# Kernel optimization log

Hardware: AMD Instinct MI355X
Metric: run time of the kernel (lower is better)

Reference implementation:

```python
import jax, jax.numpy as jnp
import numpy as np

B, CIN, COUT, K, ADIM, H, W = 32, 64, 64, 3, 64, 128, 128
PAD = K // 2


def setup_inputs() -> dict:
    key = jax.random.key(0)
    ks = jax.random.split(key, 8)
    s = lambda fan: 1.0 / np.sqrt(fan)
    return {
        "x": jax.random.normal(ks[0], (B, CIN, H, W), dtype=jnp.float32),
        "base_w": jax.random.uniform(ks[1], (COUT, CIN, K, K), minval=-s(CIN * K * K), maxval=s(CIN * K * K), dtype=jnp.float32),
        "base_b": jax.random.uniform(ks[2], (COUT,), minval=-s(CIN * K * K), maxval=s(CIN * K * K), dtype=jnp.float32),
        "w1": jax.random.uniform(ks[3], (CIN, ADIM), minval=-s(CIN), maxval=s(CIN), dtype=jnp.float32),
        "b1": jax.random.uniform(ks[4], (ADIM,), minval=-s(CIN), maxval=s(CIN), dtype=jnp.float32),
        "w2": jax.random.uniform(ks[5], (ADIM, COUT * CIN * K * K), minval=-s(ADIM), maxval=s(ADIM), dtype=jnp.float32),
        "b2": jax.random.uniform(ks[6], (COUT * CIN * K * K,), minval=-s(ADIM), maxval=s(ADIM), dtype=jnp.float32),
        "scale": jnp.float32(0.1),
    }


def reference(x, base_w, base_b, w1, b1, w2, b2, scale):
    # adaptation net: global avg pool -> MLP -> tanh
    pooled = jnp.mean(x, axis=(2, 3))                              # [B, Cin]
    h = jax.nn.relu(pooled @ w1 + b1)                              # [B, adim]
    a = jnp.tanh(h @ w2 + b2).reshape(B, COUT, CIN, K, K)          # [B,Cout,Cin,K,K]
    adapted = base_w[None] + scale * a                             # per-sample weights

    def conv_one(xi, wi):
        # xi: [Cin,H,W], wi: [Cout,Cin,K,K]
        out = jax.lax.conv_general_dilated(
            xi[None], wi, window_strides=(1, 1),
            padding=[(PAD, PAD), (PAD, PAD)],
            dimension_numbers=("NCHW", "OIHW", "NCHW"))
        return out[0]

    y = jax.vmap(conv_one)(x, adapted)                             # [B,Cout,H,W]
    return y + base_b[None, :, None, None]
```

## Files before the change

### kernel.cpp

```cpp
#include <hip/hip_runtime.h>

typedef __attribute__((ext_vector_type(8))) short short8;
typedef __attribute__((ext_vector_type(4))) float f32x4;

#define NB    32
#define CINC  64
#define COUTC 64
#define HWDIM 128
#define NPIX  16384
#define XT_H  130
#define ADIMC 64
#define WTOT  36864

#define ROWB  8320
#define ROWP  9216

__device__ inline unsigned short f2bf(float f) {
    unsigned int u = __float_as_uint(f);
    u += 0x7FFF + ((u >> 16) & 1);
    return (unsigned short)(u >> 16);
}

__device__ inline void gload_lds16(const void* g, void* l) {
    __builtin_amdgcn_global_load_lds(
        (__attribute__((address_space(1))) void*)g,
        (__attribute__((address_space(3))) void*)l, 16, 0, 0);
}

__global__ __launch_bounds__(256) void prep_kernel(
        const float* __restrict__ x, float* __restrict__ partial,
        unsigned short* __restrict__ xt) {
    __shared__ float lds[CINC][128];
    const int b = blockIdx.y, hrow = blockIdx.x, t = threadIdx.x;

    #pragma unroll
    for (int it = 0; it < 8; ++it) {
        const int c  = (t >> 5) + it * 8;
        const int w4 = (t & 31) * 4;
        f32x4 v = *(const f32x4*)(x + (((size_t)b * CINC + c) * HWDIM + hrow) * HWDIM + w4);
        *(f32x4*)&lds[c][w4 ^ (it << 2)] = v;
        float s = v[0] + v[1] + v[2] + v[3];
        for (int off = 16; off > 0; off >>= 1) s += __shfl_down(s, off, 32);
        if ((t & 31) == 0) partial[((size_t)b * HWDIM + hrow) * CINC + c] = s;
    }
    __syncthreads();

    for (int q = t; q < 1024; q += 256) {
        const int w = q >> 3, cg = (q & 7) * 8;
        const int xorc = (q & 7) << 2;
        short8 o;
        #pragma unroll
        for (int i = 0; i < 8; ++i) o[i] = (short)f2bf(lds[cg + i][w ^ xorc]);
        *(short8*)(xt + ((((size_t)b * 2 + (cg >> 5)) * XT_H + hrow + 1) * XT_H + (w + 1)) * 32
                      + (cg & 31)) = o;
    }

    if (hrow == 0) {
        for (int kc = 0; kc < 2; ++kc) {
            unsigned int* r0 = (unsigned int*)(xt + ((size_t)(b * 2 + kc) * XT_H) * XT_H * 32);
            for (int i = t; i < XT_H * 32 / 2; i += 256) r0[i] = 0u;
        }
    }
    if (hrow == HWDIM - 1) {
        for (int kc = 0; kc < 2; ++kc) {
            unsigned int* r129 = (unsigned int*)(xt + (((size_t)(b * 2 + kc) * XT_H) + 129) * XT_H * 32);
            for (int i = t; i < XT_H * 32 / 2; i += 256) r129[i] = 0u;
        }
    }
    if (t < 64) {
        const int kc = (t >> 4) & 1, wcol = (t >= 32) ? 129 : 0, i = t & 15;
        unsigned int* p = (unsigned int*)(xt + ((((size_t)(b * 2 + kc) * XT_H) + hrow + 1) * XT_H + wcol) * 32);
        p[i] = 0u;
    }
}

__global__ __launch_bounds__(256) void mlp1_kernel(
        const float* __restrict__ partial, const float* __restrict__ w1,
        const float* __restrict__ b1, float* __restrict__ hout) {
    __shared__ float red[256];
    __shared__ float pooled_s[CINC];
    const int b = blockIdx.x, t = threadIdx.x;
    const int c = t & 63, q = t >> 6;
    float s = 0.0f;
    for (int r = 0; r < 32; ++r)
        s += partial[((size_t)b * HWDIM + q * 32 + r) * CINC + c];
    red[t] = s;
    __syncthreads();
    if (t < 64)
        pooled_s[t] = (red[t] + red[t + 64] + red[t + 128] + red[t + 192]) * (1.0f / NPIX);
    __syncthreads();
    if (t < 64) {
        const int j = t;
        float acc = b1[j];
        for (int k = 0; k < CINC; ++k)
            acc = fmaf(pooled_s[k], w1[k * ADIMC + j], acc);
        hout[b * ADIMC + j] = fmaxf(acc, 0.0f);
    }
}

__global__ __launch_bounds__(320) void adapt_kernel(
        const float* __restrict__ hin, const float* __restrict__ w2,
        const float* __restrict__ b2, const float* __restrict__ base_w,
        const float* __restrict__ scale_p, unsigned short* __restrict__ adp) {
    __shared__ float lh[NB * ADIMC];
    __shared__ unsigned short lo[288 * 33];
    const int t = threadIdx.x, blk = blockIdx.x;
    for (int i = t; i < NB * ADIMC; i += 320) lh[i] = hin[i];
    __syncthreads();
    const float sc = scale_p[0];

    if (t < 288) {
        const int j = blk * 288 + t;
        float acc[NB];
        #pragma unroll
        for (int b = 0; b < NB; ++b) acc[b] = 0.0f;
        for (int k = 0; k < ADIMC; ++k) {
            const float wv = w2[(size_t)k * WTOT + j];
            #pragma unroll
            for (int b = 0; b < NB; ++b) acc[b] = fmaf(lh[b * ADIMC + k], wv, acc[b]);
        }
        const float bw = base_w[j], bb = b2[j];
        #pragma unroll
        for (int b = 0; b < NB; ++b) {
            const float val = bw + sc * tanhf(acc[b] + bb);
            lo[t * 33 + b] = f2bf(val);
        }
    }
    __syncthreads();

    const int co = blk >> 1, kc = blk & 1;
    const int mi = co >> 4, lmv = co & 15;
    for (int o = t; o < 9216; o += 320) {
        const int bb = o / 288;
        const int rem = o - bb * 288;
        const int e = rem >> 5, ci = rem & 31;
        const int hi = ci >> 3, j8 = ci & 7;
        adp[(((((size_t)bb * 9 + e) * 2 + kc) * 4 + mi) * 64 + hi * 16 + lmv) * 8 + j8]
            = lo[(ci * 9 + e) * 33 + bb];
    }
}

__global__ __launch_bounds__(256, 3) void conv_kernel(
        const unsigned short* __restrict__ xt, const unsigned short* __restrict__ adp,
        const float* __restrict__ base_b, float* __restrict__ out) {
    __shared__ __align__(1024) char smem[4 * ROWP];
    const int b = blockIdx.y, tile = blockIdx.x, t = threadIdx.x;
    const int wv = t >> 6, lane = t & 63, lm = lane & 15, lq = lane >> 4;
    const int hrow = tile * 2 + (wv >> 1);
    const int wc = (wv & 1) * 64;
    const int r0w = wv >> 1;

    f32x4 acc[4][4];
    #pragma unroll
    for (int mi = 0; mi < 4; ++mi)
        #pragma unroll
        for (int ni = 0; ni < 4; ++ni) acc[mi][ni] = (f32x4){0.f, 0.f, 0.f, 0.f};

    char* ldsrow = smem + wv * ROWP;

    for (int kc = 0; kc < 2; ++kc) {
        if (kc) __syncthreads();

        {
            const char* srow = (const char*)xt
                + ((size_t)(b * 2 + kc) * XT_H + tile * 2 + wv) * ROWB;
            #pragma unroll
            for (int k = 0; k < 9; ++k) {
                const int y  = k * 1024 + (lane << 4);
                const int sw = y ^ (((y >> 7) & 3) << 4);
                gload_lds16(srow + sw, ldsrow + k * 1024);
            }
        }
        __syncthreads();

        const unsigned short* Akc = adp + (((size_t)b * 18 + kc) << 11);
        #pragma unroll
        for (int e = 0; e < 9; ++e) {
            const int ky = e / 3, kx = e % 3;
            const unsigned short* Ae = Akc + ((size_t)e << 12);
            short8 Af[4], Bf[4];
            #pragma unroll
            for (int mi = 0; mi < 4; ++mi)
                Af[mi] = *(const short8*)(Ae + ((mi * 64 + lane) << 3));
            const int rbase = (r0w + ky) * ROWP;
            #pragma unroll
            for (int ni = 0; ni < 4; ++ni) {
                const int xr = ((wc + lm + ni * 16 + kx) << 6) + (lq << 4);
                Bf[ni] = *(const short8*)(smem + rbase + (xr ^ (((xr >> 7) & 3) << 4)));
            }
            #pragma unroll
            for (int mi = 0; mi < 4; ++mi)
                #pragma unroll
                for (int ni = 0; ni < 4; ++ni)
                    acc[mi][ni] = __builtin_amdgcn_mfma_f32_16x16x32_bf16(
                        Af[mi], Bf[ni], acc[mi][ni], 0, 0, 0);
        }
    }

    const int pixbase = hrow * HWDIM + wc + lm;
    #pragma unroll
    for (int mi = 0; mi < 4; ++mi) {
        #pragma unroll
        for (int r = 0; r < 4; ++r) {
            const int cout = mi * 16 + lq * 4 + r;
            const float bb = base_b[cout];
            #pragma unroll
            for (int ni = 0; ni < 4; ++ni)
                out[((size_t)(b * COUTC + cout) << 14) + pixbase + ni * 16] = acc[mi][ni][r] + bb;
        }
    }
}

extern "C" void kernel_launch(void* const* d_in, const int* in_sizes, int n_in,
                              void* d_out, int out_size, void* d_ws, size_t ws_size,
                              hipStream_t stream) {
    const float* x      = (const float*)d_in[0];
    const float* base_w = (const float*)d_in[1];
    const float* base_b = (const float*)d_in[2];
    const float* w1     = (const float*)d_in[3];
    const float* b1     = (const float*)d_in[4];
    const float* w2     = (const float*)d_in[5];
    const float* b2     = (const float*)d_in[6];
    const float* scale  = (const float*)d_in[7];
    float* out = (float*)d_out;

    unsigned short* xt  = (unsigned short*)d_ws;
    unsigned short* adp = (unsigned short*)((char*)d_ws + 69222400);
    float* partial      = (float*)((char*)d_ws + 71581696);
    float* hbuf         = (float*)((char*)d_ws + 72630272);

    prep_kernel<<<dim3(HWDIM, NB), 256, 0, stream>>>(x, partial, xt);
    mlp1_kernel<<<NB, 256, 0, stream>>>(partial, w1, b1, hbuf);
    adapt_kernel<<<128, 320, 0, stream>>>(hbuf, w2, b2, base_w, scale, adp);
    conv_kernel<<<dim3(64, NB), 256, 0, stream>>>(xt, adp, base_b, out);
}
```

Baseline: 326.2 us.

## Double-buffer conv channel halves in LDS, prefetch weights, remap block order

The conv kernel now stages both input-channel halves into a doubled LDS buffer up front, so the second half's global-to-LDS copy overlaps compute on the first half. It also software-pipelines the per-tap weight fragment loads into a two-slot register buffer, and remaps the 1D grid so consecutive blocks spread across batches (an XCD-style swizzle). The cost is double the LDS per block and occupancy lowered from 3 to 2 blocks per CU.

```diff
diff --git a/kernel.cpp b/kernel.cpp
--- a/kernel.cpp
+++ b/kernel.cpp
@@ -140,61 +140,77 @@
     }
 }
 
-__global__ __launch_bounds__(256, 3) void conv_kernel(
+__global__ __launch_bounds__(256, 2) void conv_kernel(
         const unsigned short* __restrict__ xt, const unsigned short* __restrict__ adp,
         const float* __restrict__ base_b, float* __restrict__ out) {
-    __shared__ __align__(1024) char smem[4 * ROWP];
-    const int b = blockIdx.y, tile = blockIdx.x, t = threadIdx.x;
+    __shared__ __align__(1024) char smem[8 * ROWP];
+    const int id = blockIdx.x, t = threadIdx.x;
+    const int j  = ((id & 7) << 8) + (id >> 3);
+    const int b  = j >> 6, tile = j & 63;
     const int wv = t >> 6, lane = t & 63, lm = lane & 15, lq = lane >> 4;
     const int hrow = tile * 2 + (wv >> 1);
     const int wc = (wv & 1) * 64;
     const int r0w = wv >> 1;
 
+    auto stage = [&](int kc) {
+        const char* srow = (const char*)xt
+            + ((size_t)(b * 2 + kc) * XT_H + tile * 2 + wv) * ROWB;
+        char* dst = smem + (kc * 4 + wv) * ROWP;
+        #pragma unroll
+        for (int k = 0; k < 9; ++k) {
+            const int y  = k * 1024 + (lane << 4);
+            const int sw = y ^ (((y >> 7) & 3) << 4);
+            gload_lds16(srow + sw, dst + k * 1024);
+        }
+    };
+
     f32x4 acc[4][4];
     #pragma unroll
     for (int mi = 0; mi < 4; ++mi)
         #pragma unroll
         for (int ni = 0; ni < 4; ++ni) acc[mi][ni] = (f32x4){0.f, 0.f, 0.f, 0.f};
 
-    char* ldsrow = smem + wv * ROWP;
-
-    for (int kc = 0; kc < 2; ++kc) {
-        if (kc) __syncthreads();
-
-        {
-            const char* srow = (const char*)xt
-                + ((size_t)(b * 2 + kc) * XT_H + tile * 2 + wv) * ROWB;
-            #pragma unroll
-            for (int k = 0; k < 9; ++k) {
-                const int y  = k * 1024 + (lane << 4);
-                const int sw = y ^ (((y >> 7) & 3) << 4);
-                gload_lds16(srow + sw, ldsrow + k * 1024);
-            }
-        }
-        __syncthreads();
-
-        const unsigned short* Akc = adp + (((size_t)b * 18 + kc) << 11);
-        #pragma unroll
-        for (int e = 0; e < 9; ++e) {
-            const int ky = e / 3, kx = e % 3;
-            const unsigned short* Ae = Akc + ((size_t)e << 12);
-            short8 Af[4], Bf[4];
+    stage(0);
+    __syncthreads();
+    stage(1);
+
+    short8 Af[2][4], Bf[4];
+
+    #pragma unroll
+    for (int s = 0; s < 18; ++s) {
+        const int kc = s / 9, e = s - kc * 9;
+        const int ky = e / 3, kx = e % 3;
+        const int slot = s & 1;
+
+        if (s == 0) {
+            const unsigned short* A0 = adp + (((size_t)b * 9) << 12);
             #pragma unroll
             for (int mi = 0; mi < 4; ++mi)
-                Af[mi] = *(const short8*)(Ae + ((mi * 64 + lane) << 3));
-            const int rbase = (r0w + ky) * ROWP;
-            #pragma unroll
-            for (int ni = 0; ni < 4; ++ni) {
-                const int xr = ((wc + lm + ni * 16 + kx) << 6) + (lq << 4);
-                Bf[ni] = *(const short8*)(smem + rbase + (xr ^ (((xr >> 7) & 3) << 4)));
-            }
+                Af[0][mi] = *(const short8*)(A0 + ((mi * 64 + lane) << 3));
+        }
+        if (s == 9) __syncthreads();
+
+        if (s + 1 < 18) {
+            const int kn = (s + 1) / 9, en = (s + 1) - kn * 9;
+            const unsigned short* An = adp + (((size_t)(b * 9 + en) * 2 + kn) << 11);
             #pragma unroll
             for (int mi = 0; mi < 4; ++mi)
-                #pragma unroll
-                for (int ni = 0; ni < 4; ++ni)
-                    acc[mi][ni] = __builtin_amdgcn_mfma_f32_16x16x32_bf16(
-                        Af[mi], Bf[ni], acc[mi][ni], 0, 0, 0);
-        }
+                Af[slot ^ 1][mi] = *(const short8*)(An + ((mi * 64 + lane) << 3));
+        }
+
+        const int rbase = (kc * 4 + r0w + ky) * ROWP;
+        #pragma unroll
+        for (int ni = 0; ni < 4; ++ni) {
+            const int xr = ((wc + lm + ni * 16 + kx) << 6) + (lq << 4);
+            Bf[ni] = *(const short8*)(smem + rbase + (xr ^ (((xr >> 7) & 3) << 4)));
+        }
+
+        #pragma unroll
+        for (int mi = 0; mi < 4; ++mi)
+            #pragma unroll
+            for (int ni = 0; ni < 4; ++ni)
+                acc[mi][ni] = __builtin_amdgcn_mfma_f32_16x16x32_bf16(
+                    Af[slot][mi], Bf[ni], acc[mi][ni], 0, 0, 0);
     }
 
     const int pixbase = hrow * HWDIM + wc + lm;
@@ -232,5 +248,5 @@
     prep_kernel<<<dim3(HWDIM, NB), 256, 0, stream>>>(x, partial, xt);
     mlp1_kernel<<<NB, 256, 0, stream>>>(partial, w1, b1, hbuf);
     adapt_kernel<<<128, 320, 0, stream>>>(hbuf, w2, b2, base_w, scale, adp);
-    conv_kernel<<<dim3(64, NB), 256, 0, stream>>>(xt, adp, base_b, out);
-}
+    conv_kernel<<<2048, 256, 0, stream>>>(xt, adp, base_b, out);
+}
```

Result: slower. 338.1 us (+3.7%).
